# Performance work log

Hardware: AMD Instinct MI355X
Metric: run time of the kernel (lower is better)

## Reference

```python
import jax, jax.numpy as jnp
import numpy as np

TEMPERATURE = 3.0
TOP_K = 5
NEG_FILL = -1e9  # matches torch fill of -1000000000.0
EPS = 1e-12      # F.normalize default eps


def setup_inputs() -> dict:
    key = jax.random.key(0)
    k1, k2 = jax.random.split(key)
    K, B, N, D = 6, 128, 65536, 256
    part_features = jax.random.normal(k1, (K, B, D), dtype=jnp.float32)
    memory_bank = jax.random.normal(k2, (K, N, D), dtype=jnp.float32)
    return {"part_features": part_features, "memory_bank": memory_bank}


def reference(part_features, memory_bank):
    K, B, D = part_features.shape
    N = memory_bank.shape[1]
    # F.normalize(features, dim=1): x / max(||x||_2, eps)
    norm = jnp.linalg.norm(part_features, axis=-1, keepdims=True)
    feats = part_features / jnp.maximum(norm, EPS)
    # sim[k] = feats[k] @ memory[k].T  -> [K, B, N]
    sim = jnp.einsum('kbd,knd->kbn', feats, memory_bank)
    # top-k filter: keep top-k per row, set the rest to -1e9 (scatter-based mask,
    # faithful to torch.topk + scatter_)
    _, idx = jax.lax.top_k(sim, TOP_K)  # idx: [K, B, TOP_K]
    mask = jnp.zeros(sim.shape, dtype=bool).at[
        jnp.arange(K)[:, None, None], jnp.arange(B)[None, :, None], idx
    ].set(True)
    filtered = jnp.where(mask, sim, NEG_FILL)
    soft_labels = jax.nn.softmax(filtered / TEMPERATURE, axis=-1)
    # soft_labels are detached in the original (no grad flows through them)
    soft_labels = jax.lax.stop_gradient(soft_labels)
    return soft_labels, sim
```

## Files before the change

### kernel.cpp

```cpp
#include <hip/hip_runtime.h>
#include <stdint.h>


#define KP 6
#define BROWS 128
#define NCOLS 65536
#define DDIM 256
#define BN 128
#define BK 32
#define NBLK (NCOLS / BN)
#define T1 512

typedef short bf16x8 __attribute__((ext_vector_type(8)));
typedef float f32x4 __attribute__((ext_vector_type(4)));

__device__ __forceinline__ uint32_t f2bf(float f) {
  uint32_t u = __float_as_uint(f);
  return (u + 0x7FFFu + ((u >> 16) & 1u)) >> 16;
}
__device__ __forceinline__ float bf2f(uint32_t h) { return __uint_as_float(h << 16); }

__device__ __forceinline__ unsigned long long mkkey(float v, uint32_t idx) {
  uint32_t u = __float_as_uint(v);
  uint32_t ov = ((int32_t)u < 0) ? ~u : (u | 0x80000000u);
  return ((unsigned long long)ov << 32) | (uint32_t)(~idx);
}
__device__ __forceinline__ float keyval(unsigned long long k) {
  uint32_t ov = (uint32_t)(k >> 32);
  uint32_t u = (ov & 0x80000000u) ? (ov ^ 0x80000000u) : ~ov;
  return __uint_as_float(u);
}
__device__ __forceinline__ uint32_t keyidx(unsigned long long k) { return ~(uint32_t)k; }

__device__ __forceinline__ void ins5(unsigned long long* t, unsigned long long key) {
  if (key > t[4]) {
    t[4] = key;
#pragma unroll
    for (int q = 4; q > 0; --q)
      if (t[q] > t[q - 1]) { unsigned long long tmp = t[q]; t[q] = t[q - 1]; t[q - 1] = tmp; }
  }
}

__device__ __forceinline__ int ldsOff(int row, int colByte) {
  return (row << 6) + (colByte ^ (((row >> 1) & 3) << 4));
}

__global__ __launch_bounds__(256) void norm_split(const float* __restrict__ part,
                                                  uint16_t* __restrict__ ahi,
                                                  uint16_t* __restrict__ alo) {
  int row = blockIdx.x;
  int t = threadIdx.x;
  float x = part[(size_t)row * DDIM + t];
  float ss = x * x;
#pragma unroll
  for (int off = 32; off; off >>= 1) ss += __shfl_down(ss, off, 64);
  __shared__ float wsum[4];
  __shared__ float nrm;
  if ((t & 63) == 0) wsum[t >> 6] = ss;
  __syncthreads();
  if (t == 0) nrm = fmaxf(sqrtf(wsum[0] + wsum[1] + wsum[2] + wsum[3]), 1e-12f);
  __syncthreads();
  float xf = x / nrm;
  uint32_t h = f2bf(xf);
  uint32_t l = f2bf(xf - bf2f(h));
  ahi[(size_t)row * DDIM + t] = (uint16_t)h;
  alo[(size_t)row * DDIM + t] = (uint16_t)l;
}

__global__ __launch_bounds__(T1, 8) void gemm_topk(const float* __restrict__ memB,
                                                   const uint16_t* __restrict__ ahi,
                                                   const uint16_t* __restrict__ alo,
                                                   float* __restrict__ soft,
                                                   float* __restrict__ sim,
                                                   unsigned long long* __restrict__ cand) {
  __shared__ __align__(16) char smem[32768];
  char* AH = smem;
  char* AL = smem + 8192;
  char* BH = smem + 16384;
  char* BL = smem + 24576;

  const int k = blockIdx.y;
  const int nb = blockIdx.x;
  const int n0 = nb * BN;
  const int tid = threadIdx.x;
  const int lane = tid & 63;
  const int wv = tid >> 6;
  const int wm = wv >> 2;
  const int wn = wv & 3;
  const int l15 = lane & 15;
  const int lq = lane >> 4;

  const float* Bbase = memB + ((size_t)k * NCOLS + n0) * DDIM;
  const uint16_t* AHg = ahi + (size_t)k * BROWS * DDIM;
  const uint16_t* ALg = alo + (size_t)k * BROWS * DDIM;

  f32x4 acc[4][2];
#pragma unroll
  for (int mf = 0; mf < 4; ++mf)
#pragma unroll
    for (int nf = 0; nf < 2; ++nf) acc[mf][nf] = (f32x4)(0.0f);

  float4 rb[2];
  uint4 rah, ral;

  auto loadChunk = [&](int c) {
#pragma unroll
    for (int p = 0; p < 2; ++p) {
      int e = (p * T1 + tid) * 4;
      int r = e >> 5, cl = e & 31;
      rb[p] = *(const float4*)(Bbase + (size_t)r * DDIM + c * BK + cl);
    }
    {
      int r = tid >> 2, cl = (tid & 3) * 8;
      rah = *(const uint4*)(AHg + (size_t)r * DDIM + c * BK + cl);
      ral = *(const uint4*)(ALg + (size_t)r * DDIM + c * BK + cl);
    }
  };

  auto storeStage = [&]() {
#pragma unroll
    for (int p = 0; p < 2; ++p) {
      int e = (p * T1 + tid) * 4;
      int r = e >> 5, cl = e & 31;
      uint32_t h0 = f2bf(rb[p].x), h1 = f2bf(rb[p].y), h2 = f2bf(rb[p].z), h3 = f2bf(rb[p].w);
      uint32_t l0 = f2bf(rb[p].x - bf2f(h0));
      uint32_t l1 = f2bf(rb[p].y - bf2f(h1));
      uint32_t l2 = f2bf(rb[p].z - bf2f(h2));
      uint32_t l3 = f2bf(rb[p].w - bf2f(h3));
      int off = ldsOff(r, cl * 2);
      *(uint2*)(BH + off) = make_uint2(h0 | (h1 << 16), h2 | (h3 << 16));
      *(uint2*)(BL + off) = make_uint2(l0 | (l1 << 16), l2 | (l3 << 16));
    }
    {
      int r = tid >> 2, cl = (tid & 3) * 8;
      int off = ldsOff(r, cl * 2);
      *(uint4*)(AH + off) = rah;
      *(uint4*)(AL + off) = ral;
    }
  };

  loadChunk(0);
#pragma unroll
  for (int c = 0; c < 8; ++c) {
    if (c) __syncthreads();
    storeStage();
    __syncthreads();
    if (c < 7) loadChunk(c + 1);
    bf16x8 afh[4], afl[4], bfh[2], bfl[2];
    int cb = lq * 16;
#pragma unroll
    for (int mf = 0; mf < 4; ++mf) {
      int r = wm * 64 + mf * 16 + l15;
      afh[mf] = *(const bf16x8*)(AH + ldsOff(r, cb));
      afl[mf] = *(const bf16x8*)(AL + ldsOff(r, cb));
    }
#pragma unroll
    for (int nf = 0; nf < 2; ++nf) {
      int r = wn * 32 + nf * 16 + l15;
      bfh[nf] = *(const bf16x8*)(BH + ldsOff(r, cb));
      bfl[nf] = *(const bf16x8*)(BL + ldsOff(r, cb));
    }
#pragma unroll
    for (int mf = 0; mf < 4; ++mf)
#pragma unroll
      for (int nf = 0; nf < 2; ++nf) {
        acc[mf][nf] = __builtin_amdgcn_mfma_f32_16x16x32_bf16(afh[mf], bfh[nf], acc[mf][nf], 0, 0, 0);
        acc[mf][nf] = __builtin_amdgcn_mfma_f32_16x16x32_bf16(afh[mf], bfl[nf], acc[mf][nf], 0, 0, 0);
        acc[mf][nf] = __builtin_amdgcn_mfma_f32_16x16x32_bf16(afl[mf], bfh[nf], acc[mf][nf], 0, 0, 0);
      }
  }

#pragma unroll
  for (int mf = 0; mf < 4; ++mf)
#pragma unroll
    for (int nf = 0; nf < 2; ++nf)
#pragma unroll
      for (int j = 0; j < 4; ++j) {
        int row = wm * 64 + mf * 16 + lq * 4 + j;
        int ccol = wn * 32 + nf * 16 + l15;
        sim[(size_t)(k * BROWS + row) * NCOLS + n0 + ccol] = acc[mf][nf][j];
      }
  {
    const size_t softbase = (size_t)(k * BROWS) * NCOLS + n0;
    float4 z4 = make_float4(0.f, 0.f, 0.f, 0.f);
#pragma unroll
    for (int p = 0; p < 8; ++p) {
      int e = (p * T1 + tid) * 4;
      int r = e >> 7, ccol = e & 127;
      *(float4*)(soft + softbase + (size_t)r * NCOLS + ccol) = z4;
    }
  }

  __syncthreads();
  unsigned long long* CAND = (unsigned long long*)smem;
#pragma unroll
  for (int mf = 0; mf < 4; ++mf) {
#pragma unroll
    for (int j = 0; j < 4; ++j) {
      int row = wm * 64 + mf * 16 + lq * 4 + j;
      unsigned long long k0 = mkkey(acc[mf][0][j], (uint32_t)(n0 + wn * 32 + l15));
      unsigned long long k1 = mkkey(acc[mf][1][j], (uint32_t)(n0 + wn * 32 + 16 + l15));
      unsigned long long w0, w1, w2, w3, w4;
#pragma unroll
      for (int rd = 0; rd < 5; ++rd) {
        unsigned long long km = k0 > k1 ? k0 : k1;
#pragma unroll
        for (int s = 1; s < 16; s <<= 1) {
          unsigned long long o = __shfl_xor(km, s, 64);
          if (o > km) km = o;
        }
        if (rd == 0) w0 = km; else if (rd == 1) w1 = km; else if (rd == 2) w2 = km;
        else if (rd == 3) w3 = km; else w4 = km;
        if (k0 == km) k0 = 0; else if (k1 == km) k1 = 0;
      }
      if (l15 == 0) {
        unsigned long long* dst = &CAND[(row * 4 + wn) * 5];
        dst[0] = w0; dst[1] = w1; dst[2] = w2; dst[3] = w3; dst[4] = w4;
      }
    }
  }
  __syncthreads();
  if (tid < BROWS) {
    unsigned long long m[5] = {0, 0, 0, 0, 0};
#pragma unroll
    for (int g = 0; g < 4; ++g)
#pragma unroll
      for (int j = 0; j < 5; ++j) ins5(m, CAND[(tid * 4 + g) * 5 + j]);
    size_t cb = ((size_t)(k * BROWS + tid) * NBLK + nb) * 5;
#pragma unroll
    for (int j = 0; j < 5; ++j) cand[cb + j] = m[j];
  }
}

__global__ __launch_bounds__(256) void topk_softmax(const unsigned long long* __restrict__ cand,
                                                    float* __restrict__ soft) {
  int row = blockIdx.x;
  const unsigned long long* cb = cand + (size_t)row * NBLK * 5;
  unsigned long long t5[5] = {0, 0, 0, 0, 0};
  for (int i = threadIdx.x; i < NBLK * 5; i += 256) ins5(t5, cb[i]);
  __shared__ unsigned long long lds[256 * 5];
#pragma unroll
  for (int j = 0; j < 5; ++j) lds[threadIdx.x * 5 + j] = t5[j];
  __syncthreads();
  if (threadIdx.x < 64) {
    unsigned long long m[5] = {0, 0, 0, 0, 0};
#pragma unroll
    for (int g = 0; g < 4; ++g)
#pragma unroll
      for (int j = 0; j < 5; ++j) ins5(m, lds[(threadIdx.x * 4 + g) * 5 + j]);
#pragma unroll
    for (int off = 1; off < 64; off <<= 1) {
      unsigned long long o[5];
#pragma unroll
      for (int j = 0; j < 5; ++j) o[j] = __shfl_xor(m[j], off, 64);
      unsigned long long out[5];
      int a = 0, b2 = 0;
#pragma unroll
      for (int r = 0; r < 5; ++r) out[r] = (m[a] >= o[b2]) ? m[a++] : o[b2++];
#pragma unroll
      for (int j = 0; j < 5; ++j) m[j] = out[j];
    }
    if (threadIdx.x == 0) {
      float v[5]; uint32_t ix[5];
#pragma unroll
      for (int j = 0; j < 5; ++j) { v[j] = keyval(m[j]); ix[j] = keyidx(m[j]); }
      float mx = v[0];
      float e[5], Z = 0.f;
#pragma unroll
      for (int j = 0; j < 5; ++j) { e[j] = expf((v[j] - mx) * (1.0f / 3.0f)); Z += e[j]; }
      float invZ = 1.0f / Z;
#pragma unroll
      for (int j = 0; j < 5; ++j) soft[(size_t)row * NCOLS + ix[j]] = e[j] * invZ;
    }
  }
}

extern "C" void kernel_launch(void* const* d_in, const int* in_sizes, int n_in,
                              void* d_out, int out_size, void* d_ws, size_t ws_size,
                              hipStream_t stream) {
  const float* part = (const float*)d_in[0];
  const float* memB = (const float*)d_in[1];
  float* soft = (float*)d_out;
  float* sim = soft + (size_t)KP * BROWS * NCOLS;

  uint16_t* ahi = (uint16_t*)d_ws;
  uint16_t* alo = ahi + (size_t)KP * BROWS * DDIM;
  unsigned long long* cand =
      (unsigned long long*)((char*)d_ws + (size_t)2 * KP * BROWS * DDIM * sizeof(uint16_t));

  norm_split<<<KP * BROWS, 256, 0, stream>>>(part, ahi, alo);
  dim3 g1(NBLK, KP);
  gemm_topk<<<g1, T1, 0, stream>>>(memB, ahi, alo, soft, sim, cand);
  topk_softmax<<<KP * BROWS, 256, 0, stream>>>(cand, soft);
}
```

Baseline: 886.5 us.

## Halve GEMM N-tile to 64 with 256 threads and reorganize candidate layout

After: 957.0 us. 1.08x slower.

```diff
diff --git a/kernel.cpp b/kernel.cpp
--- a/kernel.cpp
+++ b/kernel.cpp
@@ -6,10 +6,10 @@
 #define BROWS 128
 #define NCOLS 65536
 #define DDIM 256
-#define BN 128
+#define BN 64
 #define BK 32
 #define NBLK (NCOLS / BN)
-#define T1 512
+#define T1 256
 
 typedef short bf16x8 __attribute__((ext_vector_type(8)));
 typedef float f32x4 __attribute__((ext_vector_type(4)));
@@ -67,17 +67,17 @@
   alo[(size_t)row * DDIM + t] = (uint16_t)l;
 }
 
-__global__ __launch_bounds__(T1, 8) void gemm_topk(const float* __restrict__ memB,
+__global__ __launch_bounds__(T1, 4) void gemm_topk(const float* __restrict__ memB,
                                                    const uint16_t* __restrict__ ahi,
                                                    const uint16_t* __restrict__ alo,
                                                    float* __restrict__ soft,
                                                    float* __restrict__ sim,
                                                    unsigned long long* __restrict__ cand) {
-  __shared__ __align__(16) char smem[32768];
+  __shared__ __align__(16) char smem[24576];
   char* AH = smem;
   char* AL = smem + 8192;
   char* BH = smem + 16384;
-  char* BL = smem + 24576;
+  char* BL = smem + 20480;
 
   const int k = blockIdx.y;
   const int nb = blockIdx.x;
@@ -85,8 +85,8 @@
   const int tid = threadIdx.x;
   const int lane = tid & 63;
   const int wv = tid >> 6;
-  const int wm = wv >> 2;
-  const int wn = wv & 3;
+  const int wm = wv >> 1;
+  const int wn = wv & 1;
   const int l15 = lane & 15;
   const int lq = lane >> 4;
 
@@ -101,27 +101,29 @@
     for (int nf = 0; nf < 2; ++nf) acc[mf][nf] = (f32x4)(0.0f);
 
   float4 rb[2];
-  uint4 rah, ral;
+  uint4 rah[2], ral[2];
 
   auto loadChunk = [&](int c) {
 #pragma unroll
     for (int p = 0; p < 2; ++p) {
-      int e = (p * T1 + tid) * 4;
-      int r = e >> 5, cl = e & 31;
+      int idx = p * T1 + tid;
+      int r = idx >> 3, cl = (idx & 7) * 4;
       rb[p] = *(const float4*)(Bbase + (size_t)r * DDIM + c * BK + cl);
     }
-    {
-      int r = tid >> 2, cl = (tid & 3) * 8;
-      rah = *(const uint4*)(AHg + (size_t)r * DDIM + c * BK + cl);
-      ral = *(const uint4*)(ALg + (size_t)r * DDIM + c * BK + cl);
+#pragma unroll
+    for (int p = 0; p < 2; ++p) {
+      int idx = p * T1 + tid;
+      int r = idx >> 2, cl = (idx & 3) * 8;
+      rah[p] = *(const uint4*)(AHg + (size_t)r * DDIM + c * BK + cl);
+      ral[p] = *(const uint4*)(ALg + (size_t)r * DDIM + c * BK + cl);
     }
   };
 
   auto storeStage = [&]() {
 #pragma unroll
     for (int p = 0; p < 2; ++p) {
-      int e = (p * T1 + tid) * 4;
-      int r = e >> 5, cl = e & 31;
+      int idx = p * T1 + tid;
+      int r = idx >> 3, cl = (idx & 7) * 4;
       uint32_t h0 = f2bf(rb[p].x), h1 = f2bf(rb[p].y), h2 = f2bf(rb[p].z), h3 = f2bf(rb[p].w);
       uint32_t l0 = f2bf(rb[p].x - bf2f(h0));
       uint32_t l1 = f2bf(rb[p].y - bf2f(h1));
@@ -131,11 +133,13 @@
       *(uint2*)(BH + off) = make_uint2(h0 | (h1 << 16), h2 | (h3 << 16));
       *(uint2*)(BL + off) = make_uint2(l0 | (l1 << 16), l2 | (l3 << 16));
     }
-    {
-      int r = tid >> 2, cl = (tid & 3) * 8;
+#pragma unroll
+    for (int p = 0; p < 2; ++p) {
+      int idx = p * T1 + tid;
+      int r = idx >> 2, cl = (idx & 3) * 8;
       int off = ldsOff(r, cl * 2);
-      *(uint4*)(AH + off) = rah;
-      *(uint4*)(AL + off) = ral;
+      *(uint4*)(AH + off) = rah[p];
+      *(uint4*)(AL + off) = ral[p];
     }
   };
 
@@ -146,14 +150,8 @@
     storeStage();
     __syncthreads();
     if (c < 7) loadChunk(c + 1);
-    bf16x8 afh[4], afl[4], bfh[2], bfl[2];
-    int cb = lq * 16;
-#pragma unroll
-    for (int mf = 0; mf < 4; ++mf) {
-      int r = wm * 64 + mf * 16 + l15;
-      afh[mf] = *(const bf16x8*)(AH + ldsOff(r, cb));
-      afl[mf] = *(const bf16x8*)(AL + ldsOff(r, cb));
-    }
+    const int cb = lq * 16;
+    bf16x8 bfh[2], bfl[2];
 #pragma unroll
     for (int nf = 0; nf < 2; ++nf) {
       int r = wn * 32 + nf * 16 + l15;
@@ -161,13 +159,17 @@
       bfl[nf] = *(const bf16x8*)(BL + ldsOff(r, cb));
     }
 #pragma unroll
-    for (int mf = 0; mf < 4; ++mf)
+    for (int mf = 0; mf < 4; ++mf) {
+      int r = wm * 64 + mf * 16 + l15;
+      bf16x8 afh = *(const bf16x8*)(AH + ldsOff(r, cb));
+      bf16x8 afl = *(const bf16x8*)(AL + ldsOff(r, cb));
 #pragma unroll
       for (int nf = 0; nf < 2; ++nf) {
-        acc[mf][nf] = __builtin_amdgcn_mfma_f32_16x16x32_bf16(afh[mf], bfh[nf], acc[mf][nf], 0, 0, 0);
-        acc[mf][nf] = __builtin_amdgcn_mfma_f32_16x16x32_bf16(afh[mf], bfl[nf], acc[mf][nf], 0, 0, 0);
-        acc[mf][nf] = __builtin_amdgcn_mfma_f32_16x16x32_bf16(afl[mf], bfh[nf], acc[mf][nf], 0, 0, 0);
+        acc[mf][nf] = __builtin_amdgcn_mfma_f32_16x16x32_bf16(afh, bfh[nf], acc[mf][nf], 0, 0, 0);
+        acc[mf][nf] = __builtin_amdgcn_mfma_f32_16x16x32_bf16(afh, bfl[nf], acc[mf][nf], 0, 0, 0);
+        acc[mf][nf] = __builtin_amdgcn_mfma_f32_16x16x32_bf16(afl, bfh[nf], acc[mf][nf], 0, 0, 0);
       }
+    }
   }
 
 #pragma unroll
@@ -186,7 +188,7 @@
 #pragma unroll
     for (int p = 0; p < 8; ++p) {
       int e = (p * T1 + tid) * 4;
-      int r = e >> 7, ccol = e & 127;
+      int r = e >> 6, ccol = e & 63;
       *(float4*)(soft + softbase + (size_t)r * NCOLS + ccol) = z4;
     }
   }
@@ -214,7 +216,7 @@
         if (k0 == km) k0 = 0; else if (k1 == km) k1 = 0;
       }
       if (l15 == 0) {
-        unsigned long long* dst = &CAND[(row * 4 + wn) * 5];
+        unsigned long long* dst = &CAND[(row * 2 + wn) * 5];
         dst[0] = w0; dst[1] = w1; dst[2] = w2; dst[3] = w3; dst[4] = w4;
       }
     }
@@ -223,10 +225,10 @@
   if (tid < BROWS) {
     unsigned long long m[5] = {0, 0, 0, 0, 0};
 #pragma unroll
-    for (int g = 0; g < 4; ++g)
-#pragma unroll
-      for (int j = 0; j < 5; ++j) ins5(m, CAND[(tid * 4 + g) * 5 + j]);
-    size_t cb = ((size_t)(k * BROWS + tid) * NBLK + nb) * 5;
+    for (int g = 0; g < 2; ++g)
+#pragma unroll
+      for (int j = 0; j < 5; ++j) ins5(m, CAND[(tid * 2 + g) * 5 + j]);
+    size_t cb = ((size_t)(k * NBLK + nb) * BROWS + tid) * 5;
 #pragma unroll
     for (int j = 0; j < 5; ++j) cand[cb + j] = m[j];
   }
@@ -234,10 +236,14 @@
 
 __global__ __launch_bounds__(256) void topk_softmax(const unsigned long long* __restrict__ cand,
                                                     float* __restrict__ soft) {
-  int row = blockIdx.x;
-  const unsigned long long* cb = cand + (size_t)row * NBLK * 5;
+  int k = blockIdx.x >> 7;
+  int b = blockIdx.x & 127;
   unsigned long long t5[5] = {0, 0, 0, 0, 0};
-  for (int i = threadIdx.x; i < NBLK * 5; i += 256) ins5(t5, cb[i]);
+  for (int nb = threadIdx.x; nb < NBLK; nb += 256) {
+    const unsigned long long* p = cand + ((size_t)(k * NBLK + nb) * BROWS + b) * 5;
+#pragma unroll
+    for (int j = 0; j < 5; ++j) ins5(t5, p[j]);
+  }
   __shared__ unsigned long long lds[256 * 5];
 #pragma unroll
   for (int j = 0; j < 5; ++j) lds[threadIdx.x * 5 + j] = t5[j];
@@ -269,8 +275,9 @@
 #pragma unroll
       for (int j = 0; j < 5; ++j) { e[j] = expf((v[j] - mx) * (1.0f / 3.0f)); Z += e[j]; }
       float invZ = 1.0f / Z;
-#pragma unroll
-      for (int j = 0; j < 5; ++j) soft[(size_t)row * NCOLS + ix[j]] = e[j] * invZ;
+      size_t row = (size_t)k * BROWS + b;
+#pragma unroll
+      for (int j = 0; j < 5; ++j) soft[row * NCOLS + ix[j]] = e[j] * invZ;
     }
   }
 }
```
